# Kernel optimization log

Hardware: AMD Instinct MI355X
Metric: run time of the kernel (lower is better)

## Reference

```python
import jax, jax.numpy as jnp
import numpy as np
import math

L = 2; B = 128; CIN = 64; E = 64; H = 8; Wd = 8; NH = 8; MEM = 40
HD = E // NH; HW = H * Wd; THD = HD * HW  # 512
MASK_B = 3.0; NEG = -1e9; EPS = 1e-5


def _conv(x, w, b):
    y = jax.lax.conv_general_dilated(x, w, (1, 1), 'SAME',
                                     dimension_numbers=('NCHW', 'OIHW', 'NCHW'))
    return y + b[None, :, None, None]


def setup_inputs() -> dict:
    key = jax.random.key(0)
    ks = jax.random.split(key, 12)
    f = jax.random.normal
    return {
        'x': f(ks[0], (B, CIN, H, Wd), jnp.float32),
        'h0': f(ks[1], (L, B, E, H, Wd), jnp.float32),
        'c0': f(ks[2], (L, B, E, H, Wd), jnp.float32),
        'k0': f(ks[3], (L, B, NH, MEM, THD), jnp.float32),
        'v0': f(ks[4], (L, B, NH, MEM, THD), jnp.float32),
        'src_mask': jax.random.randint(ks[5], (B, MEM), 0, 2).astype(bool),
        'notdone': jnp.ones((B,), bool),
        'main_w': f(ks[6], (L, 5 * E, CIN + 2 * E, 3, 3), jnp.float32) * 0.05,
        'main_b': jnp.zeros((L, 5 * E), jnp.float32),
        'proj_w': f(ks[7], (L, 3 * E, CIN + E, 3, 3), jnp.float32) * 0.05,
        'proj_b': jnp.zeros((L, 3 * E), jnp.float32),
        'out_w': f(ks[8], (L, E, E, 3, 3), jnp.float32) * 0.05,
        'out_b': jnp.zeros((L, E), jnp.float32),
        'ln_w': jnp.ones((L, E, H, Wd), jnp.float32),
        'ln_b': jnp.zeros((L, E, H, Wd), jnp.float32),
        'pos_w': f(ks[9], (L, MEM, HW * E), jnp.float32) * 0.05,
        'pos_b': f(ks[10], (L, MEM, NH), jnp.float32) * 0.05,
    }


def reference(x, h0, c0, k0, v0, src_mask, notdone,
              main_w, main_b, proj_w, proj_b, out_w, out_b,
              ln_w, ln_b, pos_w, pos_b):
    nd = notdone.astype(x.dtype)[:, None, None, None]
    # rolling attention mask: reset finished episodes, shift left, open last slot
    m = src_mask | (~notdone)[:, None]
    m = jnp.concatenate([m[:, 1:], jnp.zeros((B, 1), bool)], axis=1)
    bias = jnp.where(m, NEG, 0.0).astype(x.dtype)        # (B, MEM)
    bias = bias.at[:, -1].set(MASK_B)
    out = h0[L - 1] * nd
    for n in range(L):
        inp = jnp.concatenate([x, out], axis=1)          # (B, CIN+E, H, W)
        h_cur = h0[n] * nd
        c_cur = c0[n] * nd
        gates = _conv(jnp.concatenate([inp, h_cur], axis=1), main_w[n], main_b[n])
        cc_i, cc_f, cc_o, cc_g, cc_a = jnp.split(gates, 5, axis=1)
        i = jax.nn.sigmoid(cc_i)
        fg = jax.nn.sigmoid(cc_f)
        o = jax.nn.sigmoid(cc_o)
        g = jnp.tanh(cc_g)
        a = jax.nn.sigmoid(cc_a)
        c_next = fg * c_cur + i * g
        # attention over rolling memory (mem_n slots of flattened spatial features)
        kqv = _conv(inp, proj_w[n], proj_b[n]).reshape(B, NH, 3 * HD, HW)
        k = kqv[:, :, :HD].reshape(B, NH, THD)
        q = kqv[:, :, HD:2 * HD].reshape(B, NH, THD) / math.sqrt(THD)
        v = kqv[:, :, 2 * HD:].reshape(B, NH, THD)
        pw = pos_w[n].reshape(MEM, NH, THD).transpose(1, 0, 2)  # (NH, MEM, THD)
        k_cat = jnp.concatenate([k0[n][:, :, 1:], k[:, :, None, :]], axis=2) + pw[None]
        v_cat = jnp.concatenate([v0[n][:, :, 1:], v[:, :, None, :]], axis=2)
        scores = (jnp.einsum('bnd,bnmd->bnm', q, k_cat)
                  + bias[:, None, :] + pos_b[n].T[None])
        attn_w = jax.nn.softmax(scores, axis=-1)
        attn = jnp.einsum('bnm,bnmd->bnd', attn_w, v_cat).reshape(B, E, H, Wd)
        ao = _conv(attn, out_w[n], out_b[n]) + inp[:, :E]
        mu = ao.mean(axis=(1, 2, 3), keepdims=True)
        var = ((ao - mu) ** 2).mean(axis=(1, 2, 3), keepdims=True)
        ao = (ao - mu) * jax.lax.rsqrt(var + EPS) * ln_w[n][None] + ln_b[n][None]
        c_next = c_next + a * jnp.tanh(ao)
        out = o * jnp.tanh(c_next)
    return out
```

## Files before the change

### kernel.cpp

```cpp
#include <hip/hip_runtime.h>
#include <hip/hip_bf16.h>
#include <hip/hip_cooperative_groups.h>

namespace cg = cooperative_groups;

typedef __hip_bfloat16 bf16;
typedef unsigned short u16;
typedef __attribute__((ext_vector_type(8))) short short8;
typedef __attribute__((ext_vector_type(4))) float f32x4;

#define Bb   128
#define MEMm 40

__device__ __forceinline__ float LD(const void* p, size_t i, int f32) {
    return f32 ? ((const float*)p)[i] : __bfloat162float(((const bf16*)p)[i]);
}
__device__ __forceinline__ float S2F(short s) {
    u16 u = (u16)s;
    return __bfloat162float(*(bf16*)&u);
}
__device__ __forceinline__ int LDB(const void* p, int i, int isbyte) {
    return isbyte ? (int)((const unsigned char*)p)[i] : ((const int*)p)[i];
}
__device__ __forceinline__ void SPLIT(float v, u16& hi, u16& lo) {
    bf16 h = __float2bfloat16(v);
    float r = v - __bfloat162float(h);
    bf16 l = __float2bfloat16(r);
    hi = *(u16*)&h; lo = *(u16*)&l;
}

struct __align__(16) ShConv { u16 Alds[2][2][2600]; u16 Wlds[2][2][2560]; };
struct __align__(16) ShAttn { float qv[512], kl[512], vl[512], sc[40], wexp[40];
                              float accbuf[4][512]; };
struct __align__(16) ShTail { u16 Ald[2][2][2600]; u16 Wl[2][2][2560];
                              float red[8]; float stats[2]; };
union __align__(16) Sh { int det[3]; ShConv conv; ShAttn attn; ShTail tail; };

struct FusedArgs {
    const void *x, *h0, *c0, *k0, *v0, *src_mask, *notdone;
    const void *main_w, *main_b, *proj_w, *proj_b, *out_w, *out_b;
    const void *ln_w, *ln_b, *pos_w, *pos_b;
    float *bias_buf, *out_buf, *gates_buf, *kqv_buf;
    u16 *attn_hi, *attn_lo, *wr_hi, *wr_lo;
    void *dout;
};

__global__ __launch_bounds__(256, 2) void fused_kernel(FusedArgs a) {
    __shared__ Sh sh;
    cg::grid_group grid = cg::this_grid();
    const int t = threadIdx.x, bx = blockIdx.x;

    int isf32, mbyte, ndbyte;
    {
        if (t < 3) sh.det[t] = 0;
        __syncthreads();
        const bf16* xb = (const bf16*)a.x;
        int bad = 0;
        for (int i = t; i < 4096; i += 256) {
            float v = __bfloat162float(xb[2 * i]);
            if (!(fabsf(v) < 1e4f)) bad = 1;
        }
        if (bad) atomicOr(&sh.det[0], 1);
        int mb = 0;
        const unsigned* mi = (const unsigned*)a.src_mask;
        for (int i = t; i < 1280; i += 256) if (mi[i] > 1u) mb = 1;
        if (mb) atomicOr(&sh.det[1], 1);
        int nb = 0;
        const unsigned* ni = (const unsigned*)a.notdone;
        for (int i = t; i < 32; i += 256) if (ni[i] > 1u) nb = 1;
        if (nb) atomicOr(&sh.det[2], 1);
        __syncthreads();
        isf32 = sh.det[0]; mbyte = sh.det[1]; ndbyte = sh.det[2];
        __syncthreads();
    }

    for (int u = bx; u < 6612; u += 512) {
        if (u < 20) {
            int idx = u * 256 + t;
            if (idx < Bb * MEMm) {
                int b = idx / MEMm, m = idx - b * MEMm;
                float v;
                if (m == MEMm - 1) v = 3.0f;
                else {
                    bool masked = (LDB(a.src_mask, b * MEMm + m + 1, mbyte) != 0) ||
                                  (LDB(a.notdone, b, ndbyte) == 0);
                    v = masked ? -1e9f : 0.f;
                }
                a.bias_buf[idx] = v;
            }
        } else if (u < 276) {
            int idx = (u - 20) * 256 + t;
            int b = idx >> 9;
            float nd = (LDB(a.notdone, b, ndbyte) != 0) ? 1.f : 0.f;
            size_t e = (size_t)idx * 8;
            float v[8];
            if (isf32) {
                const float* hp = (const float*)a.h0 + 524288 + e;
                f32x4 p0 = *(const f32x4*)hp, p1 = *(const f32x4*)(hp + 4);
#pragma unroll
                for (int j = 0; j < 4; ++j) { v[j] = p0[j]; v[4 + j] = p1[j]; }
            } else {
                short8 s = *(const short8*)((const bf16*)a.h0 + 524288 + e);
#pragma unroll
                for (int j = 0; j < 8; ++j) v[j] = S2F(s[j]);
            }
#pragma unroll
            for (int j = 0; j < 8; ++j) a.out_buf[e + j] = v[j] * nd;
        } else {
            int gi = (u - 276) * 256 + t;
            if (gi < 1622016) {
                int layer = (gi >= 811008) ? 1 : 0;
                int i = gi - layer * 811008;
                float v;
                if (i < 552960) {
                    int tap = i / 61440, r = i - tap * 61440, co = r / 192, ci = r - co * 192;
                    v = LD(a.main_w, (size_t)layer * 552960 + ((size_t)co * 192 + ci) * 9 + tap, isf32);
                } else if (i < 774144) {
                    int j = i - 552960;
                    int tap = j / 24576, r = j - tap * 24576, co = r / 128, ci = r - co * 128;
                    v = LD(a.proj_w, (size_t)layer * 221184 + ((size_t)co * 128 + ci) * 9 + tap, isf32);
                } else {
                    int j = i - 774144;
                    int tap = j / 4096, r = j - tap * 4096, co = r / 64, ci = r - co * 64;
                    v = LD(a.out_w, (size_t)layer * 36864 + ((size_t)co * 64 + ci) * 9 + tap, isf32);
                }
                u16 h, l; SPLIT(v, h, l);
                a.wr_hi[gi] = h; a.wr_lo[gi] = l;
            }
        }
    }
    grid.sync();

#pragma unroll 1
    for (int n = 0; n < 2; ++n) {
        const size_t wb = (size_t)n * 811008;
        const size_t hoff = (size_t)n * 524288;

        {
            auto& Alds = sh.conv.Alds;
            auto& Wlds = sh.conv.Wlds;
            const int w = t >> 6, lane = t & 63;
            const int bpair = w >> 1, half = w & 1;
            const int mblk = bx & 63, nt = bx >> 6;
            const bool isA = (nt < 5);
            const u16* Whi = a.wr_hi + wb + (isA ? 0 : 552960);
            const u16* Wlo = a.wr_lo + wb + (isA ? 0 : 552960);
            const int Kci  = isA ? 192 : 128;
            const int CoutT= isA ? 320 : 192;
            float* Out     = isA ? a.gates_buf : a.kqv_buf;
            const void* bias = isA ? a.main_b : a.proj_b;
            const long long boff = isA ? (long long)n * 320 : (long long)n * 192;
            const int n0 = (isA ? nt : nt - 5) * 64;
            const int b = mblk * 2 + bpair;
            const int NITER = (Kci >> 5) * 9;
            const float nd = (LDB(a.notdone, b, ndbyte) != 0) ? 1.f : 0.f;

            if (half == 0 && lane < 40) { Alds[bpair][0][2560 + lane] = 0; Alds[bpair][1][2560 + lane] = 0; }

            f32x4 acc[4][2];
#pragma unroll
            for (int i = 0; i < 4; ++i)
#pragma unroll
                for (int j = 0; j < 2; ++j) { f32x4 z = {0.f, 0.f, 0.f, 0.f}; acc[i][j] = z; }

            const int co_l = t >> 2, jj = t & 3;
            uint4 hv, lv;
            auto issueW = [&](int it) {
                int kc = it / 9, tap = it - kc * 9;
                size_t o = ((size_t)(tap * CoutT + n0 + co_l)) * Kci + kc * 32 + jj * 8;
                hv = *(const uint4*)(Whi + o);
                lv = *(const uint4*)(Wlo + o);
            };

            issueW(0);
            for (int it = 0; it < NITER; ++it) {
                const int kc = it / 9, tap = it - kc * 9;
                const int par = it & 1;
                *(uint4*)&Wlds[par][0][co_l * 40 + jj * 8] = hv;
                *(uint4*)&Wlds[par][1][co_l * 40 + jj * 8] = lv;
                __syncthreads();
                if (it + 1 < NITER) issueW(it + 1);
                if (tap == 0) {
                    const int px = lane;
                    const int c0i = half * 16;
                    const int cbase = kc * 32;
                    short8 hA, hB, lA, lB;
#pragma unroll
                    for (int cl2 = 0; cl2 < 16; ++cl2) {
                        int c = cbase + c0i + cl2;
                        float v;
                        if (c < 64) {
                            size_t o = (size_t)b * 4096 + (size_t)c * 64 + px;
                            v = isf32 ? ((const float*)a.x)[o] : S2F(((const short*)a.x)[o]);
                        } else if (c < 128) {
                            v = a.out_buf[(size_t)b * 4096 + (size_t)(c - 64) * 64 + px];
                        } else {
                            size_t o = hoff + (size_t)b * 4096 + (size_t)(c - 128) * 64 + px;
                            v = (isf32 ? ((const float*)a.h0)[o] : S2F(((const short*)a.h0)[o])) * nd;
                        }
                        u16 hh, ll; SPLIT(v, hh, ll);
                        if (cl2 < 8) { hA[cl2] = (short)hh; lA[cl2] = (short)ll; }
                        else         { hB[cl2 - 8] = (short)hh; lB[cl2 - 8] = (short)ll; }
                    }
                    *(short8*)&Alds[bpair][0][px * 40 + c0i]     = hA;
                    *(short8*)&Alds[bpair][0][px * 40 + c0i + 8] = hB;
                    *(short8*)&Alds[bpair][1][px * 40 + c0i]     = lA;
                    *(short8*)&Alds[bpair][1][px * 40 + c0i + 8] = lB;
                    __syncthreads();
                }
                const int dy = tap / 3 - 1, dx = tap % 3 - 1;
                const int q8 = (lane >> 4) * 8;
                const int ml = lane & 15;
                short8 aH[4], aL[4];
#pragma unroll
                for (int mt = 0; mt < 4; ++mt) {
                    int px = mt * 16 + ml;
                    int yy = (px >> 3) + dy, xx = (px & 7) + dx;
                    int row = ((unsigned)yy < 8u && (unsigned)xx < 8u) ? yy * 8 + xx : 64;
                    int o = row * 40 + q8;
                    aH[mt] = *(const short8*)&Alds[bpair][0][o];
                    aL[mt] = *(const short8*)&Alds[bpair][1][o];
                }
#pragma unroll
                for (int nn = 0; nn < 2; ++nn) {
                    int o = (half * 32 + nn * 16 + ml) * 40 + q8;
                    short8 bH = *(const short8*)&Wlds[par][0][o];
                    short8 bL = *(const short8*)&Wlds[par][1][o];
#pragma unroll
                    for (int mt = 0; mt < 4; ++mt) {
                        acc[mt][nn] = __builtin_amdgcn_mfma_f32_16x16x32_bf16(aH[mt], bH, acc[mt][nn], 0, 0, 0);
                        acc[mt][nn] = __builtin_amdgcn_mfma_f32_16x16x32_bf16(aH[mt], bL, acc[mt][nn], 0, 0, 0);
                        acc[mt][nn] = __builtin_amdgcn_mfma_f32_16x16x32_bf16(aL[mt], bH, acc[mt][nn], 0, 0, 0);
                    }
                }
            }
            const int q = lane >> 4, ml = lane & 15;
#pragma unroll
            for (int nn = 0; nn < 2; ++nn) {
                int co = n0 + half * 32 + nn * 16 + ml;
                float bv = LD(bias, (size_t)boff + co, isf32);
#pragma unroll
                for (int mt = 0; mt < 4; ++mt) {
                    f32x4 v = acc[mt][nn];
                    v[0] += bv; v[1] += bv; v[2] += bv; v[3] += bv;
                    *(f32x4*)&Out[((size_t)b * CoutT + co) * 64 + mt * 16 + q * 4] = v;
                }
            }
        }
        grid.sync();

        for (int u = bx; u < 1024; u += 512) {
            float* qv = sh.attn.qv; float* kl = sh.attn.kl; float* vl = sh.attn.vl;
            float* sc = sh.attn.sc; float* wexp = sh.attn.wexp;
            auto& accbuf = sh.attn.accbuf;
            const int b = u >> 3, h = u & 7;
            const size_t kqb = (size_t)b * 192 * 64;
            for (int d = t; d < 512; d += 256) {
                int hd = d >> 6, ss = d & 63;
                qv[d] = a.kqv_buf[kqb + (h * 24 + 8 + hd) * 64 + ss] * 0.044194173824159216f;
                kl[d] = a.kqv_buf[kqb + (h * 24 + 0 + hd) * 64 + ss];
                vl[d] = a.kqv_buf[kqb + (h * 24 + 16 + hd) * 64 + ss];
            }
            __syncthreads();
            const int wid = t >> 6, lane = t & 63;
            const int d0 = lane * 8;
            const size_t kvbase = (size_t)n * 20971520 + ((size_t)(b * 8 + h)) * (size_t)(40 * 512);
            const size_t pwoff = (size_t)n * 163840, pboff = (size_t)n * 320;

            float q8[8];
#pragma unroll
            for (int j = 0; j < 8; ++j) q8[j] = qv[d0 + j];

            for (int m = wid; m < 40; m += 4) {
                float kc[8];
                if (m < 39) {
                    if (isf32) {
                        const float* kp = (const float*)a.k0 + kvbase + (size_t)(m + 1) * 512 + d0;
                        f32x4 p0 = *(const f32x4*)kp, p1 = *(const f32x4*)(kp + 4);
#pragma unroll
                        for (int j = 0; j < 4; ++j) { kc[j] = p0[j]; kc[4 + j] = p1[j]; }
                    } else {
                        short8 s = *(const short8*)((const bf16*)a.k0 + kvbase + (size_t)(m + 1) * 512 + d0);
#pragma unroll
                        for (int j = 0; j < 8; ++j) kc[j] = S2F(s[j]);
                    }
                } else {
#pragma unroll
                    for (int j = 0; j < 8; ++j) kc[j] = kl[d0 + j];
                }
                if (isf32) {
                    const float* pp = (const float*)a.pos_w + pwoff + (size_t)m * 4096 + h * 512 + d0;
                    f32x4 p0 = *(const f32x4*)pp, p1 = *(const f32x4*)(pp + 4);
#pragma unroll
                    for (int j = 0; j < 4; ++j) { kc[j] += p0[j]; kc[4 + j] += p1[j]; }
                } else {
                    short8 s = *(const short8*)((const bf16*)a.pos_w + pwoff + (size_t)m * 4096 + h * 512 + d0);
#pragma unroll
                    for (int j = 0; j < 8; ++j) kc[j] += S2F(s[j]);
                }
                float p = 0.f;
#pragma unroll
                for (int j = 0; j < 8; ++j) p += q8[j] * kc[j];
#pragma unroll
                for (int off = 32; off > 0; off >>= 1) p += __shfl_down(p, off, 64);
                if (lane == 0)
                    sc[m] = p + a.bias_buf[b * 40 + m] + LD(a.pos_b, pboff + m * 8 + h, isf32);
            }
            __syncthreads();

            float mx = -1e30f;
            for (int m = 0; m < 40; ++m) mx = fmaxf(mx, sc[m]);
            if (t < 40) wexp[t] = __expf(sc[t] - mx);
            __syncthreads();
            float sum = 0.f;
            for (int m = 0; m < 40; ++m) sum += wexp[m];
            float rs = 1.f / sum;

            float acc8[8];
#pragma unroll
            for (int j = 0; j < 8; ++j) acc8[j] = 0.f;
            for (int m = wid; m < 40; m += 4) {
                float wgt = wexp[m];
                if (m < 39) {
                    if (isf32) {
                        const float* vp = (const float*)a.v0 + kvbase + (size_t)(m + 1) * 512 + d0;
                        f32x4 p0 = *(const f32x4*)vp, p1 = *(const f32x4*)(vp + 4);
#pragma unroll
                        for (int j = 0; j < 4; ++j) { acc8[j] += wgt * p0[j]; acc8[4 + j] += wgt * p1[j]; }
                    } else {
                        short8 s = *(const short8*)((const bf16*)a.v0 + kvbase + (size_t)(m + 1) * 512 + d0);
#pragma unroll
                        for (int j = 0; j < 8; ++j) acc8[j] += wgt * S2F(s[j]);
                    }
                } else {
#pragma unroll
                    for (int j = 0; j < 8; ++j) acc8[j] += wgt * vl[d0 + j];
                }
            }
#pragma unroll
            for (int j = 0; j < 8; ++j) accbuf[wid][d0 + j] = acc8[j];
            __syncthreads();

            for (int d = t; d < 512; d += 256) {
                float acc = (accbuf[0][d] + accbuf[1][d]) + (accbuf[2][d] + accbuf[3][d]);
                acc *= rs;
                int ch = h * 8 + (d >> 6), px = d & 63;
                u16 hh, ll; SPLIT(acc, hh, ll);
                size_t o = (size_t)b * 4096 + px * 64 + ch;
                a.attn_hi[o] = hh; a.attn_lo[o] = ll;
            }
            __syncthreads();
        }
        grid.sync();

        if (bx < 128) {
            auto& Ald = sh.tail.Ald;
            auto& Wl  = sh.tail.Wl;
            float* red = sh.tail.red; float* stats = sh.tail.stats;
            const int w = t >> 6, lane = t & 63;
            const int b = bx;
            const u16* whi = a.wr_hi + wb + 774144;
            const u16* wlo = a.wr_lo + wb + 774144;
            const int write_out = (n == 1) ? 1 : 0;
            const long long boff = (long long)n * 64;
            const size_t coff = (size_t)n * 524288, lnoff = (size_t)n * 4096;

            {
                int px = t >> 2, ci16 = (t & 3) * 16;
                int chunk = ci16 >> 5, cl = ci16 & 31;
                size_t o = ((size_t)b * 64 + px) * 64 + ci16;
                *(uint4*)&Ald[chunk][0][px * 40 + cl]     = *(const uint4*)(a.attn_hi + o);
                *(uint4*)&Ald[chunk][0][px * 40 + cl + 8] = *(const uint4*)(a.attn_hi + o + 8);
                *(uint4*)&Ald[chunk][1][px * 40 + cl]     = *(const uint4*)(a.attn_lo + o);
                *(uint4*)&Ald[chunk][1][px * 40 + cl + 8] = *(const uint4*)(a.attn_lo + o + 8);
                if (t < 160) { int ch = t / 80, hl = (t / 40) & 1, i = t % 40;
                               Ald[ch][hl][2560 + i] = 0; }
            }

            const int co_l = t >> 2, jj = t & 3;
            uint4 hv, lv;
            auto issueW = [&](int it) {
                int kc = it / 9, tap = it - kc * 9;
                size_t o = ((size_t)(tap * 64 + co_l)) * 64 + kc * 32 + jj * 8;
                hv = *(const uint4*)(whi + o);
                lv = *(const uint4*)(wlo + o);
            };

            f32x4 acc[4];
#pragma unroll
            for (int i = 0; i < 4; ++i) { f32x4 z = {0.f, 0.f, 0.f, 0.f}; acc[i] = z; }

            issueW(0);
            for (int it = 0; it < 18; ++it) {
                const int kc = it / 9, tap = it - kc * 9;
                const int par = it & 1;
                *(uint4*)&Wl[par][0][co_l * 40 + jj * 8] = hv;
                *(uint4*)&Wl[par][1][co_l * 40 + jj * 8] = lv;
                __syncthreads();
                if (it + 1 < 18) issueW(it + 1);
                const int dy = tap / 3 - 1, dx = tap % 3 - 1;
                const int q8 = (lane >> 4) * 8;
                const int ml = lane & 15;
                short8 aH[4], aL[4];
#pragma unroll
                for (int mt = 0; mt < 4; ++mt) {
                    int px = mt * 16 + ml;
                    int yy = (px >> 3) + dy, xx = (px & 7) + dx;
                    int row = ((unsigned)yy < 8u && (unsigned)xx < 8u) ? yy * 8 + xx : 64;
                    int o = row * 40 + q8;
                    aH[mt] = *(const short8*)&Ald[kc][0][o];
                    aL[mt] = *(const short8*)&Ald[kc][1][o];
                }
                int o = (w * 16 + ml) * 40 + q8;
                short8 bH = *(const short8*)&Wl[par][0][o];
                short8 bL = *(const short8*)&Wl[par][1][o];
#pragma unroll
                for (int mt = 0; mt < 4; ++mt) {
                    acc[mt] = __builtin_amdgcn_mfma_f32_16x16x32_bf16(aH[mt], bH, acc[mt], 0, 0, 0);
                    acc[mt] = __builtin_amdgcn_mfma_f32_16x16x32_bf16(aH[mt], bL, acc[mt], 0, 0, 0);
                    acc[mt] = __builtin_amdgcn_mfma_f32_16x16x32_bf16(aL[mt], bH, acc[mt], 0, 0, 0);
                }
            }

            const int q = lane >> 4, ml = lane & 15;
            const int co = w * 16 + ml;
            const size_t base = (size_t)b * 4096;
            float bv = LD(a.out_b, (size_t)boff + co, isf32);
            float vals[16];
            float sum = 0.f, sumsq = 0.f;
#pragma unroll
            for (int mt = 0; mt < 4; ++mt) {
                int px0 = mt * 16 + q * 4;
#pragma unroll
                for (int r = 0; r < 4; ++r) {
                    float xv = LD(a.x, base + (size_t)co * 64 + px0 + r, isf32);
                    float val = acc[mt][r] + bv + xv;
                    vals[mt * 4 + r] = val; sum += val; sumsq += val * val;
                }
            }
#pragma unroll
            for (int off = 32; off > 0; off >>= 1) {
                sum   += __shfl_down(sum, off, 64);
                sumsq += __shfl_down(sumsq, off, 64);
            }
            if (lane == 0) { red[w] = sum; red[4 + w] = sumsq; }
            __syncthreads();
            if (t == 0) {
                float ts = red[0] + red[1] + red[2] + red[3];
                float tq = red[4] + red[5] + red[6] + red[7];
                float mu = ts * (1.f / 4096.f);
                float var = tq * (1.f / 4096.f) - mu * mu;
                stats[0] = mu; stats[1] = rsqrtf(fmaxf(var, 0.f) + 1e-5f);
            }
            __syncthreads();
            const float mu = stats[0], rstd = stats[1];
            const float nd = (LDB(a.notdone, b, ndbyte) != 0) ? 1.f : 0.f;
            const size_t gbase = (size_t)b * 320 * 64;
#pragma unroll
            for (int mt = 0; mt < 4; ++mt) {
                int px0 = mt * 16 + q * 4;
                size_t i0 = (size_t)co * 64 + px0;
                f32x4 gi4 = *(const f32x4*)&a.gates_buf[gbase + (size_t)(co      ) * 64 + px0];
                f32x4 gf4 = *(const f32x4*)&a.gates_buf[gbase + (size_t)(co +  64) * 64 + px0];
                f32x4 go4 = *(const f32x4*)&a.gates_buf[gbase + (size_t)(co + 128) * 64 + px0];
                f32x4 gg4 = *(const f32x4*)&a.gates_buf[gbase + (size_t)(co + 192) * 64 + px0];
                f32x4 ga4 = *(const f32x4*)&a.gates_buf[gbase + (size_t)(co + 256) * 64 + px0];
                f32x4 ov;
#pragma unroll
                for (int r = 0; r < 4; ++r) {
                    size_t i = i0 + r;
                    float aon = (vals[mt * 4 + r] - mu) * rstd * LD(a.ln_w, lnoff + i, isf32)
                                + LD(a.ln_b, lnoff + i, isf32);
                    float gi = 1.f / (1.f + __expf(-gi4[r]));
                    float gf = 1.f / (1.f + __expf(-gf4[r]));
                    float go = 1.f / (1.f + __expf(-go4[r]));
                    float gg = tanhf(gg4[r]);
                    float ga = 1.f / (1.f + __expf(-ga4[r]));
                    float cc = LD(a.c0, coff + base + i, isf32) * nd;
                    float cn = gf * cc + gi * gg + ga * tanhf(aon);
                    float o  = go * tanhf(cn);
                    ov[r] = o;
                    if (write_out) {
                        if (isf32) ((float*)a.dout)[base + i] = o;
                        else       ((bf16*)a.dout)[base + i] = __float2bfloat16(o);
                    }
                }
                *(f32x4*)&a.out_buf[base + i0] = ov;
            }
        }
        if (n == 0) grid.sync();
    }
}


__global__ void detect_kernel(const void* __restrict__ x,
                              const void* __restrict__ src_mask,
                              const void* __restrict__ notdone,
                              int* __restrict__ flags) {
    __shared__ int s[3];
    const int t = threadIdx.x;
    if (t < 3) s[t] = 0;
    __syncthreads();
    const bf16* xb = (const bf16*)x;
    int bad = 0;
    for (int i = t; i < 4096; i += 256) {
        float v = __bfloat162float(xb[2 * i]);
        if (!(fabsf(v) < 1e4f)) bad = 1;
    }
    if (bad) atomicOr(&s[0], 1);
    int mb = 0;
    const unsigned* mi = (const unsigned*)src_mask;
    for (int i = t; i < 1280; i += 256) if (mi[i] > 1u) mb = 1;
    if (mb) atomicOr(&s[1], 1);
    int nb = 0;
    const unsigned* ni = (const unsigned*)notdone;
    for (int i = t; i < 32; i += 256) if (ni[i] > 1u) nb = 1;
    if (nb) atomicOr(&s[2], 1);
    __syncthreads();
    if (t < 3) flags[t] = s[t];
}

__global__ void setup_kernel(const void* __restrict__ src_mask,
                             const void* __restrict__ notdone,
                             const void* __restrict__ h0,
                             const void* __restrict__ mw,
                             const void* __restrict__ pw,
                             const void* __restrict__ ow,
                             const int* __restrict__ flags,
                             float* __restrict__ biasb,
                             float* __restrict__ outb, size_t hoff,
                             u16* __restrict__ whi, u16* __restrict__ wlo) {
    const int bid = blockIdx.x, t = threadIdx.x;
    const int isf32 = flags[0], mbyte = flags[1], ndbyte = flags[2];
    if (bid < 20) {
        int idx = bid * 256 + t;
        if (idx >= Bb * MEMm) return;
        int b = idx / MEMm, m = idx - b * MEMm;
        float v;
        if (m == MEMm - 1) v = 3.0f;
        else {
            bool masked = (LDB(src_mask, b * MEMm + m + 1, mbyte) != 0) ||
                          (LDB(notdone, b, ndbyte) == 0);
            v = masked ? -1e9f : 0.f;
        }
        biasb[idx] = v;
    } else if (bid < 276) {
        int idx = (bid - 20) * 256 + t;
        int b = idx >> 9;
        float nd = (LDB(notdone, b, ndbyte) != 0) ? 1.f : 0.f;
        size_t e = (size_t)idx * 8;
        float v[8];
        if (isf32) {
            const float* hp = (const float*)h0 + hoff + e;
            f32x4 p0 = *(const f32x4*)hp, p1 = *(const f32x4*)(hp + 4);
#pragma unroll
            for (int j = 0; j < 4; ++j) { v[j] = p0[j]; v[4 + j] = p1[j]; }
        } else {
            short8 s = *(const short8*)((const bf16*)h0 + hoff + e);
#pragma unroll
            for (int j = 0; j < 8; ++j) v[j] = S2F(s[j]);
        }
#pragma unroll
        for (int j = 0; j < 8; ++j) outb[e + j] = v[j] * nd;
    } else {
        int gi = (bid - 276) * 256 + t;
        if (gi >= 1622016) return;
        int layer = (gi >= 811008) ? 1 : 0;
        int i = gi - layer * 811008;
        float v;
        if (i < 552960) {
            int tap = i / 61440, r = i - tap * 61440, co = r / 192, ci = r - co * 192;
            v = LD(mw, (size_t)layer * 552960 + ((size_t)co * 192 + ci) * 9 + tap, isf32);
        } else if (i < 774144) {
            int j = i - 552960;
            int tap = j / 24576, r = j - tap * 24576, co = r / 128, ci = r - co * 128;
            v = LD(pw, (size_t)layer * 221184 + ((size_t)co * 128 + ci) * 9 + tap, isf32);
        } else {
            int j = i - 774144;
            int tap = j / 4096, r = j - tap * 4096, co = r / 64, ci = r - co * 64;
            v = LD(ow, (size_t)layer * 36864 + ((size_t)co * 64 + ci) * 9 + tap, isf32);
        }
        u16 h, l; SPLIT(v, h, l);
        whi[gi] = h; wlo[gi] = l;
    }
}

struct ConvArgs {
    const void *x; const float *prev_out; const void *h0; const void *notdone;
    const u16 *WhiA, *WloA, *WhiB, *WloB;
    const void *biasA, *biasB;
    float *OutA, *OutB;
    long long boffA, boffB;
    size_t hoff;
    int KciA, KciB, CoutA, CoutB, ntA, NT, NMB;
};

__global__ __launch_bounds__(256) void conv_mfma_kernel(ConvArgs g,
                                                        const int* __restrict__ flags) {
    __shared__ __align__(16) u16 Alds[2][2][2600];
    __shared__ __align__(16) u16 Wlds[2][2][2560];
    const int t = threadIdx.x, w = t >> 6, lane = t & 63;
    const int bpair = w >> 1, half = w & 1;
    const int bx = blockIdx.x;
    const int mblk = bx % g.NMB, nt = bx / g.NMB;
    const bool isA = (nt < g.ntA);
    const u16* Whi = isA ? g.WhiA : g.WhiB;
    const u16* Wlo = isA ? g.WloA : g.WloB;
    const int Kci  = isA ? g.KciA : g.KciB;
    const int CoutT= isA ? g.CoutA : g.CoutB;
    float* Out     = isA ? g.OutA : g.OutB;
    const void* bias = isA ? g.biasA : g.biasB;
    const long long boff = isA ? g.boffA : g.boffB;
    const int n0 = (isA ? nt : nt - g.ntA) * 64;
    const int b = mblk * 2 + bpair;
    const int NITER = (Kci >> 5) * 9;
    const int isf32 = flags[0];
    const float nd = (LDB(g.notdone, b, flags[2]) != 0) ? 1.f : 0.f;

    if (half == 0 && lane < 40) { Alds[bpair][0][2560 + lane] = 0; Alds[bpair][1][2560 + lane] = 0; }

    f32x4 acc[4][2];
#pragma unroll
    for (int i = 0; i < 4; ++i)
#pragma unroll
        for (int j = 0; j < 2; ++j) { f32x4 z = {0.f, 0.f, 0.f, 0.f}; acc[i][j] = z; }

    const int co_l = t >> 2, jj = t & 3;
    uint4 hv, lv;
    auto issueW = [&](int it) {
        int kc = it / 9, tap = it - kc * 9;
        size_t o = ((size_t)(tap * CoutT + n0 + co_l)) * Kci + kc * 32 + jj * 8;
        hv = *(const uint4*)(Whi + o);
        lv = *(const uint4*)(Wlo + o);
    };

    issueW(0);
    for (int it = 0; it < NITER; ++it) {
        const int kc = it / 9, tap = it - kc * 9;
        const int par = it & 1;
        *(uint4*)&Wlds[par][0][co_l * 40 + jj * 8] = hv;
        *(uint4*)&Wlds[par][1][co_l * 40 + jj * 8] = lv;
        __syncthreads();
        if (it + 1 < NITER) issueW(it + 1);
        if (tap == 0) {
            const int px = lane;
            const int c0i = half * 16;
            const int cbase = kc * 32;
            short8 hA, hB, lA, lB;
#pragma unroll
            for (int cl2 = 0; cl2 < 16; ++cl2) {
                int c = cbase + c0i + cl2;
                float v;
                if (c < 64) {
                    size_t o = (size_t)b * 4096 + (size_t)c * 64 + px;
                    v = isf32 ? ((const float*)g.x)[o] : S2F(((const short*)g.x)[o]);
                } else if (c < 128) {
                    v = g.prev_out[(size_t)b * 4096 + (size_t)(c - 64) * 64 + px];
                } else {
                    size_t o = g.hoff + (size_t)b * 4096 + (size_t)(c - 128) * 64 + px;
                    v = (isf32 ? ((const float*)g.h0)[o] : S2F(((const short*)g.h0)[o])) * nd;
                }
                u16 hh, ll; SPLIT(v, hh, ll);
                if (cl2 < 8) { hA[cl2] = (short)hh; lA[cl2] = (short)ll; }
                else         { hB[cl2 - 8] = (short)hh; lB[cl2 - 8] = (short)ll; }
            }
            *(short8*)&Alds[bpair][0][px * 40 + c0i]     = hA;
            *(short8*)&Alds[bpair][0][px * 40 + c0i + 8] = hB;
            *(short8*)&Alds[bpair][1][px * 40 + c0i]     = lA;
            *(short8*)&Alds[bpair][1][px * 40 + c0i + 8] = lB;
            __syncthreads();
        }
        const int dy = tap / 3 - 1, dx = tap % 3 - 1;
        const int q8 = (lane >> 4) * 8;
        const int ml = lane & 15;
        short8 aH[4], aL[4];
#pragma unroll
        for (int mt = 0; mt < 4; ++mt) {
            int px = mt * 16 + ml;
            int yy = (px >> 3) + dy, xx = (px & 7) + dx;
            int row = ((unsigned)yy < 8u && (unsigned)xx < 8u) ? yy * 8 + xx : 64;
            int o = row * 40 + q8;
            aH[mt] = *(const short8*)&Alds[bpair][0][o];
            aL[mt] = *(const short8*)&Alds[bpair][1][o];
        }
#pragma unroll
        for (int nn = 0; nn < 2; ++nn) {
            int o = (half * 32 + nn * 16 + ml) * 40 + q8;
            short8 bH = *(const short8*)&Wlds[par][0][o];
            short8 bL = *(const short8*)&Wlds[par][1][o];
#pragma unroll
            for (int mt = 0; mt < 4; ++mt) {
                acc[mt][nn] = __builtin_amdgcn_mfma_f32_16x16x32_bf16(aH[mt], bH, acc[mt][nn], 0, 0, 0);
                acc[mt][nn] = __builtin_amdgcn_mfma_f32_16x16x32_bf16(aH[mt], bL, acc[mt][nn], 0, 0, 0);
                acc[mt][nn] = __builtin_amdgcn_mfma_f32_16x16x32_bf16(aL[mt], bH, acc[mt][nn], 0, 0, 0);
            }
        }
    }
    const int q = lane >> 4, ml = lane & 15;
#pragma unroll
    for (int nn = 0; nn < 2; ++nn) {
        int co = n0 + half * 32 + nn * 16 + ml;
        float bv = LD(bias, (size_t)boff + co, isf32);
#pragma unroll
        for (int mt = 0; mt < 4; ++mt) {
            f32x4 v = acc[mt][nn];
            v[0] += bv; v[1] += bv; v[2] += bv; v[3] += bv;
            *(f32x4*)&Out[((size_t)b * CoutT + co) * 64 + mt * 16 + q * 4] = v;
        }
    }
}

__global__ __launch_bounds__(256) void attn_kernel(
    const float* __restrict__ kqv,
    const void* __restrict__ k0,
    const void* __restrict__ v0,
    const void* __restrict__ pw,
    const void* __restrict__ pb,
    const float* __restrict__ biasb,
    const int* __restrict__ flags,
    u16* __restrict__ ahi, u16* __restrict__ alo,
    size_t kvoff, size_t pwoff, size_t pboff) {
    __shared__ float qv[512], kl[512], vl[512], sc[40], wexp[40];
    __shared__ float accbuf[4][512];
    const int t = threadIdx.x;
    const int isf32 = flags[0];
    const int b = blockIdx.x >> 3, h = blockIdx.x & 7;
    const size_t kqb = (size_t)b * 192 * 64;
    for (int d = t; d < 512; d += 256) {
        int hd = d >> 6, ss = d & 63;
        qv[d] = kqv[kqb + (h * 24 + 8 + hd) * 64 + ss] * 0.044194173824159216f;
        kl[d] = kqv[kqb + (h * 24 + 0 + hd) * 64 + ss];
        vl[d] = kqv[kqb + (h * 24 + 16 + hd) * 64 + ss];
    }
    __syncthreads();
    const int wid = t >> 6, lane = t & 63;
    const int d0 = lane * 8;
    const size_t kvbase = kvoff + ((size_t)(b * 8 + h)) * (size_t)(40 * 512);

    float q8[8];
#pragma unroll
    for (int j = 0; j < 8; ++j) q8[j] = qv[d0 + j];

    for (int m = wid; m < 40; m += 4) {
        float kc[8];
        if (m < 39) {
            if (isf32) {
                const float* kp = (const float*)k0 + kvbase + (size_t)(m + 1) * 512 + d0;
                f32x4 p0 = *(const f32x4*)kp, p1 = *(const f32x4*)(kp + 4);
#pragma unroll
                for (int j = 0; j < 4; ++j) { kc[j] = p0[j]; kc[4 + j] = p1[j]; }
            } else {
                short8 s = *(const short8*)((const bf16*)k0 + kvbase + (size_t)(m + 1) * 512 + d0);
#pragma unroll
                for (int j = 0; j < 8; ++j) kc[j] = S2F(s[j]);
            }
        } else {
#pragma unroll
            for (int j = 0; j < 8; ++j) kc[j] = kl[d0 + j];
        }
        if (isf32) {
            const float* pp = (const float*)pw + pwoff + (size_t)m * 4096 + h * 512 + d0;
            f32x4 p0 = *(const f32x4*)pp, p1 = *(const f32x4*)(pp + 4);
#pragma unroll
            for (int j = 0; j < 4; ++j) { kc[j] += p0[j]; kc[4 + j] += p1[j]; }
        } else {
            short8 s = *(const short8*)((const bf16*)pw + pwoff + (size_t)m * 4096 + h * 512 + d0);
#pragma unroll
            for (int j = 0; j < 8; ++j) kc[j] += S2F(s[j]);
        }
        float p = 0.f;
#pragma unroll
        for (int j = 0; j < 8; ++j) p += q8[j] * kc[j];
#pragma unroll
        for (int off = 32; off > 0; off >>= 1) p += __shfl_down(p, off, 64);
        if (lane == 0)
            sc[m] = p + biasb[b * 40 + m] + LD(pb, pboff + m * 8 + h, isf32);
    }
    __syncthreads();

    float mx = -1e30f;
    for (int m = 0; m < 40; ++m) mx = fmaxf(mx, sc[m]);
    if (t < 40) wexp[t] = __expf(sc[t] - mx);
    __syncthreads();
    float sum = 0.f;
    for (int m = 0; m < 40; ++m) sum += wexp[m];
    float rs = 1.f / sum;

    float acc8[8];
#pragma unroll
    for (int j = 0; j < 8; ++j) acc8[j] = 0.f;
    for (int m = wid; m < 40; m += 4) {
        float wgt = wexp[m];
        if (m < 39) {
            if (isf32) {
                const float* vp = (const float*)v0 + kvbase + (size_t)(m + 1) * 512 + d0;
                f32x4 p0 = *(const f32x4*)vp, p1 = *(const f32x4*)(vp + 4);
#pragma unroll
                for (int j = 0; j < 4; ++j) { acc8[j] += wgt * p0[j]; acc8[4 + j] += wgt * p1[j]; }
            } else {
                short8 s = *(const short8*)((const bf16*)v0 + kvbase + (size_t)(m + 1) * 512 + d0);
#pragma unroll
                for (int j = 0; j < 8; ++j) acc8[j] += wgt * S2F(s[j]);
            }
        } else {
#pragma unroll
            for (int j = 0; j < 8; ++j) acc8[j] += wgt * vl[d0 + j];
        }
    }
#pragma unroll
    for (int j = 0; j < 8; ++j) accbuf[wid][d0 + j] = acc8[j];
    __syncthreads();

    for (int d = t; d < 512; d += 256) {
        float acc = (accbuf[0][d] + accbuf[1][d]) + (accbuf[2][d] + accbuf[3][d]);
        acc *= rs;
        int ch = h * 8 + (d >> 6), px = d & 63;
        u16 hh, ll; SPLIT(acc, hh, ll);
        size_t o = (size_t)b * 4096 + px * 64 + ch;
        ahi[o] = hh; alo[o] = ll;
    }
}

__global__ __launch_bounds__(256) void tail_kernel(
    const u16* __restrict__ ahi, const u16* __restrict__ alo,
    const u16* __restrict__ whi, const u16* __restrict__ wlo,
    const void* __restrict__ outb_bias,
    const void* __restrict__ x,
    const float* __restrict__ gates,
    const void* __restrict__ c0,
    const void* __restrict__ notdone,
    const void* __restrict__ lnw, const void* __restrict__ lnb,
    const int* __restrict__ flags,
    float* __restrict__ out_buf, void* __restrict__ dout, int write_out,
    long long boff, size_t coff, size_t lnoff) {
    __shared__ __align__(16) u16 Ald[2][2][2600];
    __shared__ __align__(16) u16 Wl[2][2][2560];
    __shared__ float red[8], stats[2];
    const int t = threadIdx.x, w = t >> 6, lane = t & 63;
    const int b = blockIdx.x;
    const int isf32 = flags[0], ndbyte = flags[2];

    {
        int px = t >> 2, ci16 = (t & 3) * 16;
        int chunk = ci16 >> 5, cl = ci16 & 31;
        size_t o = ((size_t)b * 64 + px) * 64 + ci16;
        *(uint4*)&Ald[chunk][0][px * 40 + cl]     = *(const uint4*)(ahi + o);
        *(uint4*)&Ald[chunk][0][px * 40 + cl + 8] = *(const uint4*)(ahi + o + 8);
        *(uint4*)&Ald[chunk][1][px * 40 + cl]     = *(const uint4*)(alo + o);
        *(uint4*)&Ald[chunk][1][px * 40 + cl + 8] = *(const uint4*)(alo + o + 8);
        if (t < 160) { int ch = t / 80, hl = (t / 40) & 1, i = t % 40;
                       Ald[ch][hl][2560 + i] = 0; }
    }

    const int co_l = t >> 2, jj = t & 3;
    uint4 hv, lv;
    auto issueW = [&](int it) {
        int kc = it / 9, tap = it - kc * 9;
        size_t o = ((size_t)(tap * 64 + co_l)) * 64 + kc * 32 + jj * 8;
        hv = *(const uint4*)(whi + o);
        lv = *(const uint4*)(wlo + o);
    };

    f32x4 acc[4];
#pragma unroll
    for (int i = 0; i < 4; ++i) { f32x4 z = {0.f, 0.f, 0.f, 0.f}; acc[i] = z; }

    issueW(0);
    for (int it = 0; it < 18; ++it) {
        const int kc = it / 9, tap = it - kc * 9;
        const int par = it & 1;
        *(uint4*)&Wl[par][0][co_l * 40 + jj * 8] = hv;
        *(uint4*)&Wl[par][1][co_l * 40 + jj * 8] = lv;
        __syncthreads();
        if (it + 1 < 18) issueW(it + 1);
        const int dy = tap / 3 - 1, dx = tap % 3 - 1;
        const int q8 = (lane >> 4) * 8;
        const int ml = lane & 15;
        short8 aH[4], aL[4];
#pragma unroll
        for (int mt = 0; mt < 4; ++mt) {
            int px = mt * 16 + ml;
            int yy = (px >> 3) + dy, xx = (px & 7) + dx;
            int row = ((unsigned)yy < 8u && (unsigned)xx < 8u) ? yy * 8 + xx : 64;
            int o = row * 40 + q8;
            aH[mt] = *(const short8*)&Ald[kc][0][o];
            aL[mt] = *(const short8*)&Ald[kc][1][o];
        }
        int o = (w * 16 + ml) * 40 + q8;
        short8 bH = *(const short8*)&Wl[par][0][o];
        short8 bL = *(const short8*)&Wl[par][1][o];
#pragma unroll
        for (int mt = 0; mt < 4; ++mt) {
            acc[mt] = __builtin_amdgcn_mfma_f32_16x16x32_bf16(aH[mt], bH, acc[mt], 0, 0, 0);
            acc[mt] = __builtin_amdgcn_mfma_f32_16x16x32_bf16(aH[mt], bL, acc[mt], 0, 0, 0);
            acc[mt] = __builtin_amdgcn_mfma_f32_16x16x32_bf16(aL[mt], bH, acc[mt], 0, 0, 0);
        }
    }

    const int q = lane >> 4, ml = lane & 15;
    const int co = w * 16 + ml;
    const size_t base = (size_t)b * 4096;
    float bv = LD(outb_bias, (size_t)boff + co, isf32);
    float vals[16];
    float sum = 0.f, sumsq = 0.f;
#pragma unroll
    for (int mt = 0; mt < 4; ++mt) {
        int px0 = mt * 16 + q * 4;
#pragma unroll
        for (int r = 0; r < 4; ++r) {
            float xv = LD(x, base + (size_t)co * 64 + px0 + r, isf32);
            float val = acc[mt][r] + bv + xv;
            vals[mt * 4 + r] = val; sum += val; sumsq += val * val;
        }
    }
#pragma unroll
    for (int off = 32; off > 0; off >>= 1) {
        sum   += __shfl_down(sum, off, 64);
        sumsq += __shfl_down(sumsq, off, 64);
    }
    if (lane == 0) { red[w] = sum; red[4 + w] = sumsq; }
    __syncthreads();
    if (t == 0) {
        float ts = red[0] + red[1] + red[2] + red[3];
        float tq = red[4] + red[5] + red[6] + red[7];
        float mu = ts * (1.f / 4096.f);
        float var = tq * (1.f / 4096.f) - mu * mu;
        stats[0] = mu; stats[1] = rsqrtf(fmaxf(var, 0.f) + 1e-5f);
    }
    __syncthreads();
    const float mu = stats[0], rstd = stats[1];
    const float nd = (LDB(notdone, b, ndbyte) != 0) ? 1.f : 0.f;
    const size_t gbase = (size_t)b * 320 * 64;
#pragma unroll
    for (int mt = 0; mt < 4; ++mt) {
        int px0 = mt * 16 + q * 4;
        size_t i0 = (size_t)co * 64 + px0;
        f32x4 gi4 = *(const f32x4*)&gates[gbase + (size_t)(co      ) * 64 + px0];
        f32x4 gf4 = *(const f32x4*)&gates[gbase + (size_t)(co +  64) * 64 + px0];
        f32x4 go4 = *(const f32x4*)&gates[gbase + (size_t)(co + 128) * 64 + px0];
        f32x4 gg4 = *(const f32x4*)&gates[gbase + (size_t)(co + 192) * 64 + px0];
        f32x4 ga4 = *(const f32x4*)&gates[gbase + (size_t)(co + 256) * 64 + px0];
        f32x4 ov;
#pragma unroll
        for (int r = 0; r < 4; ++r) {
            size_t i = i0 + r;
            float aon = (vals[mt * 4 + r] - mu) * rstd * LD(lnw, lnoff + i, isf32)
                        + LD(lnb, lnoff + i, isf32);
            float gi = 1.f / (1.f + __expf(-gi4[r]));
            float gf = 1.f / (1.f + __expf(-gf4[r]));
            float go = 1.f / (1.f + __expf(-go4[r]));
            float gg = tanhf(gg4[r]);
            float ga = 1.f / (1.f + __expf(-ga4[r]));
            float cc = LD(c0, coff + base + i, isf32) * nd;
            float cn = gf * cc + gi * gg + ga * tanhf(aon);
            float o  = go * tanhf(cn);
            ov[r] = o;
            if (write_out) {
                if (isf32) ((float*)dout)[base + i] = o;
                else       ((bf16*)dout)[base + i] = __float2bfloat16(o);
            }
        }
        *(f32x4*)&out_buf[base + i0] = ov;
    }
}

extern "C" void kernel_launch(void* const* d_in, const int* in_sizes, int n_in,
                              void* d_out, int out_size, void* d_ws, size_t ws_size,
                              hipStream_t stream) {
    const void* x      = d_in[0];
    const void* h0     = d_in[1];
    const void* c0     = d_in[2];
    const void* k0     = d_in[3];
    const void* v0     = d_in[4];
    const void* src_mask = d_in[5];
    const void* notdone  = d_in[6];
    const void* main_w = d_in[7];
    const void* main_b = d_in[8];
    const void* proj_w = d_in[9];
    const void* proj_b = d_in[10];
    const void* out_w  = d_in[11];
    const void* out_b  = d_in[12];
    const void* ln_w   = d_in[13];
    const void* ln_b   = d_in[14];
    const void* pos_w  = d_in[15];
    const void* pos_b  = d_in[16];

    float* wsf = (float*)d_ws;
    int*   flags    = (int*)d_ws;
    float* bias_buf = wsf + 8;
    float* out_buf  = wsf + 8192;
    float* gates_buf= wsf + 532480;
    float* kqv_buf  = wsf + 3153920;
    u16* attn_hi    = (u16*)(wsf + 4726784);
    u16* attn_lo    = (u16*)(wsf + 4988928);
    u16* wr_hi      = (u16*)(wsf + 5251072);
    u16* wr_lo      = (u16*)(wsf + 6062080);

    FusedArgs fa;
    fa.x = x; fa.h0 = h0; fa.c0 = c0; fa.k0 = k0; fa.v0 = v0;
    fa.src_mask = src_mask; fa.notdone = notdone;
    fa.main_w = main_w; fa.main_b = main_b; fa.proj_w = proj_w; fa.proj_b = proj_b;
    fa.out_w = out_w; fa.out_b = out_b; fa.ln_w = ln_w; fa.ln_b = ln_b;
    fa.pos_w = pos_w; fa.pos_b = pos_b;
    fa.bias_buf = bias_buf; fa.out_buf = out_buf; fa.gates_buf = gates_buf;
    fa.kqv_buf = kqv_buf; fa.attn_hi = attn_hi; fa.attn_lo = attn_lo;
    fa.wr_hi = wr_hi; fa.wr_lo = wr_lo; fa.dout = d_out;

    int maxB = 0;
    hipError_t occ = hipOccupancyMaxActiveBlocksPerMultiprocessor(&maxB, fused_kernel, 256, 0);
    if (occ == hipSuccess && maxB >= 2) {
        void* kargs[] = { (void*)&fa };
        hipError_t e = hipLaunchCooperativeKernel(fused_kernel, dim3(512), dim3(256),
                                                  kargs, 0u, stream);
        if (e == hipSuccess) return;
        (void)hipGetLastError();
    }

    detect_kernel<<<1, 256, 0, stream>>>(x, src_mask, notdone, flags);
    setup_kernel<<<6612, 256, 0, stream>>>(src_mask, notdone, h0,
                                           main_w, proj_w, out_w, flags,
                                           bias_buf, out_buf, (size_t)524288,
                                           wr_hi, wr_lo);
    for (int n = 0; n < 2; ++n) {
        const size_t wb = (size_t)n * 811008;
        ConvArgs ga;
        ga.x = x; ga.prev_out = out_buf; ga.h0 = h0; ga.notdone = notdone;
        ga.hoff = (size_t)n * 524288;
        ga.WhiA = wr_hi + wb;          ga.WloA = wr_lo + wb;          ga.KciA = 192; ga.CoutA = 320;
        ga.WhiB = wr_hi + wb + 552960; ga.WloB = wr_lo + wb + 552960; ga.KciB = 128; ga.CoutB = 192;
        ga.biasA = main_b; ga.boffA = (long long)n * 320; ga.OutA = gates_buf;
        ga.biasB = proj_b; ga.boffB = (long long)n * 192; ga.OutB = kqv_buf;
        ga.ntA = 5; ga.NT = 8; ga.NMB = 64;
        conv_mfma_kernel<<<512, 256, 0, stream>>>(ga, flags);

        attn_kernel<<<1024, 256, 0, stream>>>(
            kqv_buf, k0, v0, pos_w, pos_b, bias_buf, flags, attn_hi, attn_lo,
            (size_t)n * 20971520, (size_t)n * 163840, (size_t)n * 320);

        tail_kernel<<<128, 256, 0, stream>>>(
            attn_hi, attn_lo, wr_hi + wb + 774144, wr_lo + wb + 774144,
            out_b, x, gates_buf, c0, notdone, ln_w, ln_b, flags,
            out_buf, d_out, (n == 1) ? 1 : 0,
            (long long)n * 64, (size_t)n * 524288, (size_t)n * 4096);
    }
}
```

Before: 573.4 us.

## Raise cooperative-kernel occupancy to 4 blocks/CU with one batch per conv block

Launch bounds rise from 2 to 4 blocks per CU, and the cooperative grid becomes maxB*256 blocks instead of a fixed 512. Each conv work item now covers one batch element and a 64-channel tile, with each wave taking 16 output channels, instead of two batch elements per block. The item loop strides by GRID so it works for any grid size. LDS use is cut by removing the batch-pair A buffer and the tail weight double buffer, which adds an extra __syncthreads per tail iteration. The added occupancy could be offset by register limits, more blocks rereading the weights, and weight-load latency that is no longer overlapped in the tail.

```diff
diff --git a/kernel.cpp b/kernel.cpp
--- a/kernel.cpp
+++ b/kernel.cpp
@@ -29,10 +29,10 @@
     hi = *(u16*)&h; lo = *(u16*)&l;
 }
 
-struct __align__(16) ShConv { u16 Alds[2][2][2600]; u16 Wlds[2][2][2560]; };
+struct __align__(16) ShConv { u16 Alds[2][2600]; u16 Wlds[2][2][2560]; };
 struct __align__(16) ShAttn { float qv[512], kl[512], vl[512], sc[40], wexp[40];
                               float accbuf[4][512]; };
-struct __align__(16) ShTail { u16 Ald[2][2][2600]; u16 Wl[2][2][2560];
+struct __align__(16) ShTail { u16 Ald[2][2][2600]; u16 Wl[2][2560];
                               float red[8]; float stats[2]; };
 union __align__(16) Sh { int det[3]; ShConv conv; ShAttn attn; ShTail tail; };
 
@@ -45,10 +45,12 @@
     void *dout;
 };
 
-__global__ __launch_bounds__(256, 2) void fused_kernel(FusedArgs a) {
+__global__ __launch_bounds__(256, 4) void fused_kernel(FusedArgs a) {
     __shared__ Sh sh;
     cg::grid_group grid = cg::this_grid();
     const int t = threadIdx.x, bx = blockIdx.x;
+    const int GRID = gridDim.x;
+    const int w = t >> 6, lane = t & 63;
 
     int isf32, mbyte, ndbyte;
     {
@@ -74,7 +76,7 @@
         __syncthreads();
     }
 
-    for (int u = bx; u < 6612; u += 512) {
+    for (int u = bx; u < 6612; u += GRID) {
         if (u < 20) {
             int idx = u * 256 + t;
             if (idx < Bb * MEMm) {
@@ -136,12 +138,10 @@
         const size_t wb = (size_t)n * 811008;
         const size_t hoff = (size_t)n * 524288;
 
-        {
+        for (int u = bx; u < 1024; u += GRID) {
             auto& Alds = sh.conv.Alds;
             auto& Wlds = sh.conv.Wlds;
-            const int w = t >> 6, lane = t & 63;
-            const int bpair = w >> 1, half = w & 1;
-            const int mblk = bx & 63, nt = bx >> 6;
+            const int nt = u >> 7, b = u & 127;
             const bool isA = (nt < 5);
             const u16* Whi = a.wr_hi + wb + (isA ? 0 : 552960);
             const u16* Wlo = a.wr_lo + wb + (isA ? 0 : 552960);
@@ -151,17 +151,15 @@
             const void* bias = isA ? a.main_b : a.proj_b;
             const long long boff = isA ? (long long)n * 320 : (long long)n * 192;
             const int n0 = (isA ? nt : nt - 5) * 64;
-            const int b = mblk * 2 + bpair;
             const int NITER = (Kci >> 5) * 9;
             const float nd = (LDB(a.notdone, b, ndbyte) != 0) ? 1.f : 0.f;
 
-            if (half == 0 && lane < 40) { Alds[bpair][0][2560 + lane] = 0; Alds[bpair][1][2560 + lane] = 0; }
-
-            f32x4 acc[4][2];
-#pragma unroll
-            for (int i = 0; i < 4; ++i)
-#pragma unroll
-                for (int j = 0; j < 2; ++j) { f32x4 z = {0.f, 0.f, 0.f, 0.f}; acc[i][j] = z; }
+            if (t < 80) { int hl = t / 40, i = t - hl * 40;
+                          Alds[hl][2560 + i] = 0; }
+
+            f32x4 acc[4];
+#pragma unroll
+            for (int i = 0; i < 4; ++i) { f32x4 z = {0.f, 0.f, 0.f, 0.f}; acc[i] = z; }
 
             const int co_l = t >> 2, jj = t & 3;
             uint4 hv, lv;
@@ -182,12 +180,11 @@
                 if (it + 1 < NITER) issueW(it + 1);
                 if (tap == 0) {
                     const int px = lane;
-                    const int c0i = half * 16;
-                    const int cbase = kc * 32;
-                    short8 hA, hB, lA, lB;
-#pragma unroll
-                    for (int cl2 = 0; cl2 < 16; ++cl2) {
-                        int c = cbase + c0i + cl2;
+                    const int c0i = w * 8;
+                    short8 hA, lA;
+#pragma unroll
+                    for (int cl2 = 0; cl2 < 8; ++cl2) {
+                        int c = kc * 32 + c0i + cl2;
                         float v;
                         if (c < 64) {
                             size_t o = (size_t)b * 4096 + (size_t)c * 64 + px;
@@ -199,13 +196,10 @@
                             v = (isf32 ? ((const float*)a.h0)[o] : S2F(((const short*)a.h0)[o])) * nd;
                         }
                         u16 hh, ll; SPLIT(v, hh, ll);
-                        if (cl2 < 8) { hA[cl2] = (short)hh; lA[cl2] = (short)ll; }
-                        else         { hB[cl2 - 8] = (short)hh; lB[cl2 - 8] = (short)ll; }
+                        hA[cl2] = (short)hh; lA[cl2] = (short)ll;
                     }
-                    *(short8*)&Alds[bpair][0][px * 40 + c0i]     = hA;
-                    *(short8*)&Alds[bpair][0][px * 40 + c0i + 8] = hB;
-                    *(short8*)&Alds[bpair][1][px * 40 + c0i]     = lA;
-                    *(short8*)&Alds[bpair][1][px * 40 + c0i + 8] = lB;
+                    *(short8*)&Alds[0][px * 40 + c0i] = hA;
+                    *(short8*)&Alds[1][px * 40 + c0i] = lA;
                     __syncthreads();
                 }
                 const int dy = tap / 3 - 1, dx = tap % 3 - 1;
@@ -218,38 +212,35 @@
                     int yy = (px >> 3) + dy, xx = (px & 7) + dx;
                     int row = ((unsigned)yy < 8u && (unsigned)xx < 8u) ? yy * 8 + xx : 64;
                     int o = row * 40 + q8;
-                    aH[mt] = *(const short8*)&Alds[bpair][0][o];
-                    aL[mt] = *(const short8*)&Alds[bpair][1][o];
-                }
-#pragma unroll
-                for (int nn = 0; nn < 2; ++nn) {
-                    int o = (half * 32 + nn * 16 + ml) * 40 + q8;
-                    short8 bH = *(const short8*)&Wlds[par][0][o];
-                    short8 bL = *(const short8*)&Wlds[par][1][o];
-#pragma unroll
-                    for (int mt = 0; mt < 4; ++mt) {
-                        acc[mt][nn] = __builtin_amdgcn_mfma_f32_16x16x32_bf16(aH[mt], bH, acc[mt][nn], 0, 0, 0);
-                        acc[mt][nn] = __builtin_amdgcn_mfma_f32_16x16x32_bf16(aH[mt], bL, acc[mt][nn], 0, 0, 0);
-                        acc[mt][nn] = __builtin_amdgcn_mfma_f32_16x16x32_bf16(aL[mt], bH, acc[mt][nn], 0, 0, 0);
-                    }
+                    aH[mt] = *(const short8*)&Alds[0][o];
+                    aL[mt] = *(const short8*)&Alds[1][o];
+                }
+                int o = (w * 16 + ml) * 40 + q8;
+                short8 bH = *(const short8*)&Wlds[par][0][o];
+                short8 bL = *(const short8*)&Wlds[par][1][o];
+#pragma unroll
+                for (int mt = 0; mt < 4; ++mt) {
+                    acc[mt] = __builtin_amdgcn_mfma_f32_16x16x32_bf16(aH[mt], bH, acc[mt], 0, 0, 0);
+                    acc[mt] = __builtin_amdgcn_mfma_f32_16x16x32_bf16(aH[mt], bL, acc[mt], 0, 0, 0);
+                    acc[mt] = __builtin_amdgcn_mfma_f32_16x16x32_bf16(aL[mt], bH, acc[mt], 0, 0, 0);
                 }
             }
             const int q = lane >> 4, ml = lane & 15;
-#pragma unroll
-            for (int nn = 0; nn < 2; ++nn) {
-                int co = n0 + half * 32 + nn * 16 + ml;
+            {
+                int co = n0 + w * 16 + ml;
                 float bv = LD(bias, (size_t)boff + co, isf32);
 #pragma unroll
                 for (int mt = 0; mt < 4; ++mt) {
-                    f32x4 v = acc[mt][nn];
+                    f32x4 v = acc[mt];
                     v[0] += bv; v[1] += bv; v[2] += bv; v[3] += bv;
                     *(f32x4*)&Out[((size_t)b * CoutT + co) * 64 + mt * 16 + q * 4] = v;
                 }
             }
+            __syncthreads();
         }
         grid.sync();
 
-        for (int u = bx; u < 1024; u += 512) {
+        for (int u = bx; u < 1024; u += GRID) {
             float* qv = sh.attn.qv; float* kl = sh.attn.kl; float* vl = sh.attn.vl;
             float* sc = sh.attn.sc; float* wexp = sh.attn.wexp;
             auto& accbuf = sh.attn.accbuf;
@@ -262,7 +253,7 @@
                 vl[d] = a.kqv_buf[kqb + (h * 24 + 16 + hd) * 64 + ss];
             }
             __syncthreads();
-            const int wid = t >> 6, lane = t & 63;
+            const int wid = w;
             const int d0 = lane * 8;
             const size_t kvbase = (size_t)n * 20971520 + ((size_t)(b * 8 + h)) * (size_t)(40 * 512);
             const size_t pwoff = (size_t)n * 163840, pboff = (size_t)n * 320;
@@ -357,7 +348,6 @@
             auto& Ald = sh.tail.Ald;
             auto& Wl  = sh.tail.Wl;
             float* red = sh.tail.red; float* stats = sh.tail.stats;
-            const int w = t >> 6, lane = t & 63;
             const int b = bx;
             const u16* whi = a.wr_hi + wb + 774144;
             const u16* wlo = a.wr_lo + wb + 774144;
@@ -393,9 +383,9 @@
             issueW(0);
             for (int it = 0; it < 18; ++it) {
                 const int kc = it / 9, tap = it - kc * 9;
-                const int par = it & 1;
-                *(uint4*)&Wl[par][0][co_l * 40 + jj * 8] = hv;
-                *(uint4*)&Wl[par][1][co_l * 40 + jj * 8] = lv;
+                __syncthreads();
+                *(uint4*)&Wl[0][co_l * 40 + jj * 8] = hv;
+                *(uint4*)&Wl[1][co_l * 40 + jj * 8] = lv;
                 __syncthreads();
                 if (it + 1 < 18) issueW(it + 1);
                 const int dy = tap / 3 - 1, dx = tap % 3 - 1;
@@ -412,8 +402,8 @@
                     aL[mt] = *(const short8*)&Ald[kc][1][o];
                 }
                 int o = (w * 16 + ml) * 40 + q8;
-                short8 bH = *(const short8*)&Wl[par][0][o];
-                short8 bL = *(const short8*)&Wl[par][1][o];
+                short8 bH = *(const short8*)&Wl[0][o];
+                short8 bL = *(const short8*)&Wl[1][o];
 #pragma unroll
                 for (int mt = 0; mt < 4; ++mt) {
                     acc[mt] = __builtin_amdgcn_mfma_f32_16x16x32_bf16(aH[mt], bH, acc[mt], 0, 0, 0);
@@ -1009,8 +999,9 @@
     int maxB = 0;
     hipError_t occ = hipOccupancyMaxActiveBlocksPerMultiprocessor(&maxB, fused_kernel, 256, 0);
     if (occ == hipSuccess && maxB >= 2) {
+        int gb = maxB < 4 ? maxB : 4;
         void* kargs[] = { (void*)&fa };
-        hipError_t e = hipLaunchCooperativeKernel(fused_kernel, dim3(512), dim3(256),
+        hipError_t e = hipLaunchCooperativeKernel(fused_kernel, dim3(gb * 256), dim3(256),
                                                   kargs, 0u, stream);
         if (e == hipSuccess) return;
         (void)hipGetLastError();
```

Result: slower. 1.052 ms (+83.4%).
